# Kernel optimization log

Measured on AMD Instinct MI355X. Metric: run time of the kernel, lower is better.

The kernel has to match this reference:

```python
import jax, jax.numpy as jnp
import numpy as np

N_USERS = 100000
N_ITEMS = 50000
N_TOPICS = 1000
N_NODES = N_USERS + N_ITEMS + N_TOPICS
DIM = 64
LAYERS = 3
NNZ = 4000000
BATCH = 16384


def setup_inputs() -> dict:
    key = jax.random.key(0)
    ks = jax.random.split(key, 8)
    user_w = jax.random.normal(ks[0], (N_USERS, DIM), dtype=jnp.float32) * 0.1
    item_w = jax.random.normal(ks[1], (N_ITEMS, DIM), dtype=jnp.float32) * 0.1
    topic_w = jax.random.normal(ks[2], (N_TOPICS, DIM), dtype=jnp.float32) * 0.1
    vals = jax.random.uniform(ks[3], (NNZ,), dtype=jnp.float32)
    row = jax.random.randint(ks[4], (NNZ,), 0, N_NODES, dtype=jnp.int32)
    col = jax.random.randint(ks[5], (NNZ,), 0, N_NODES, dtype=jnp.int32)
    users = jax.random.randint(ks[6], (BATCH,), 0, N_USERS, dtype=jnp.int32)
    items = jax.random.randint(ks[7], (BATCH,), 0, N_ITEMS, dtype=jnp.int32)
    return {"user_w": user_w, "item_w": item_w, "topic_w": topic_w,
            "vals": vals, "row": row, "col": col,
            "users": users, "items": items}


def _spmm(vals, row, col, x):
    # y[r] = sum over edges e with row[e]==r of vals[e] * x[col[e]]
    msgs = vals[:, None] * x[col]  # [NNZ, DIM]
    return jax.ops.segment_sum(msgs, row, num_segments=N_NODES)


def reference(user_w, item_w, topic_w, vals, row, col, users, items):
    all_emb = jnp.concatenate([user_w, item_w, topic_w], axis=0)  # [N, D]
    acc = all_emb
    emb = all_emb
    for _ in range(LAYERS):
        emb = _spmm(vals, row, col, emb)
        acc = acc + emb
    out = acc / jnp.asarray(LAYERS + 1, dtype=acc.dtype)  # mean over stacked layers
    u = out[users]                       # [B, D] user rows
    i = out[N_USERS + items]             # [B, D] item rows (offset into node table)
    return jnp.sum(u * i, axis=1)        # [B]
```

## Files before the change

### kernel.cpp

```cpp
#include <hip/hip_runtime.h>
#include <hip/hip_fp16.h>

#define N_USERS 100000
#define N_ITEMS 50000
#define N_TOPICS 1000
#define N_NODES (N_USERS + N_ITEMS + N_TOPICS)
#define DIM 64
#define NNZ 4000000
#define BATCH 16384

#define BROWS 128
#define NB ((N_NODES + BROWS - 1) / BROWS)
#define NPART 256
#define CHUNK ((NNZ + NPART - 1) / NPART)
#define SEGCAP 4608

#define QSCALE 16384.0f
#define QINV   6.103515625e-05f

#define CONCAT_TOTAL (N_NODES * (DIM / 4))
#define CONCAT_BLOCKS ((CONCAT_TOTAL + 1023) / 1024)
#define BINIT_TOTAL (2 * BATCH * (DIM / 4))
#define BINIT_BLOCKS ((BINIT_TOTAL + 1023) / 1024)

__global__ void __launch_bounds__(1024)
phase0(const float4* __restrict__ uw,
       const float4* __restrict__ iw,
       const float4* __restrict__ tw,
       const int* __restrict__ row,
       const int* __restrict__ users,
       const int* __restrict__ items,
       __half2* __restrict__ x0,
       float4* __restrict__ accb,
       int* __restrict__ hcnt,
       int* __restrict__ sync) {
    __shared__ int h[NB];
    const int blk = blockIdx.x;
    const int t = threadIdx.x;
    if (blk < NPART) {
        if (blk == 0 && t == 0) *sync = 0;
        for (int i = t; i < NB; i += 1024) h[i] = 0;
        __syncthreads();
        int e0 = blk * CHUNK;
        int e1 = e0 + CHUNK; if (e1 > NNZ) e1 = NNZ;
        for (int e = e0 + t; e < e1; e += 1024) {
            int r = __builtin_nontemporal_load(&row[e]);
            atomicAdd(&h[r >> 7], 1);
        }
        __syncthreads();
        int* dst = hcnt + (size_t)blk * NB;
        for (int i = t; i < NB; i += 1024) dst[i] = h[i];
    } else if (blk < NPART + CONCAT_BLOCKS) {
        int tid = (blk - NPART) * 1024 + t;
        if (tid >= CONCAT_TOTAL) return;
        int node = tid >> 4;
        int q = tid & 15;
        float4 v;
        if (node < N_USERS)                v = uw[node * 16 + q];
        else if (node < N_USERS + N_ITEMS) v = iw[(node - N_USERS) * 16 + q];
        else                               v = tw[(node - N_USERS - N_ITEMS) * 16 + q];
        x0[tid * 2]     = __floats2half2_rn(v.x, v.y);
        x0[tid * 2 + 1] = __floats2half2_rn(v.z, v.w);
    } else {
        int tid = (blk - NPART - CONCAT_BLOCKS) * 1024 + t;
        if (tid >= BINIT_TOTAL) return;
        int r = tid >> 4;
        int q = tid & 15;
        float4 v;
        if (r < BATCH) v = uw[(size_t)users[r] * 16 + q];
        else           v = iw[(size_t)items[r - BATCH] * 16 + q];
        accb[tid] = v;
    }
}

__global__ void __launch_bounds__(256)
part_scanAB(int* __restrict__ hcnt,
            int* __restrict__ bcnt,
            int* __restrict__ bptr,
            int* __restrict__ rowptr,
            int* __restrict__ sync) {
    const int t = threadIdx.x;
    const int lane = t & 63;
    const int wid = t >> 6;
    int b = blockIdx.x * 4 + wid;
    int carry = 0;
    for (int base = 0; base < NPART; base += 64) {
        int g = base + lane;
        int v = hcnt[(size_t)g * NB + b];
        int x = v;
        #pragma unroll
        for (int off = 1; off < 64; off <<= 1) {
            int y = __shfl_up(x, off, 64);
            if (lane >= off) x += y;
        }
        int tot = __shfl(x, 63, 64);
        hcnt[(size_t)g * NB + b] = carry + x - v;
        carry += tot;
    }
    if (lane == 0) bcnt[b] = carry;
    __syncthreads();
    __threadfence();
    __shared__ int lastFlag;
    if (t == 0) lastFlag = (atomicAdd(sync, 1) == (int)gridDim.x - 1);
    __syncthreads();
    if (!lastFlag) return;

    __shared__ int wsum[4];
    __shared__ int carry_s;
    if (t == 0) carry_s = 0;
    __syncthreads();
    for (int base = 0; base < NB; base += 256) {
        int i = base + t;
        int v = (i < NB) ? bcnt[i] : 0;
        int x = v;
        #pragma unroll
        for (int off = 1; off < 64; off <<= 1) {
            int y = __shfl_up(x, off, 64);
            if (lane >= off) x += y;
        }
        if (lane == 63) wsum[wid] = x;
        __syncthreads();
        int wbase = 0;
        for (int w = 0; w < wid; ++w) wbase += wsum[w];
        int excl = carry_s + wbase + (x - v);
        if (i < NB) bptr[i] = excl;
        __syncthreads();
        if (t == 255) carry_s = excl + v;
        __syncthreads();
    }
    if (t == 0) { bptr[NB] = NNZ; rowptr[N_NODES] = NNZ; }
}

__global__ void __launch_bounds__(1024)
part_scatter(const int* __restrict__ row,
             const int* __restrict__ col,
             const float* __restrict__ vals,
             const int* __restrict__ hcnt,
             const int* __restrict__ bptr,
             int2* __restrict__ cvtmp) {
    __shared__ int cur[NB];
    const int g = blockIdx.x;
    const int t = threadIdx.x;
    const int* hoff = hcnt + (size_t)g * NB;
    for (int i = t; i < NB; i += 1024) cur[i] = bptr[i] + hoff[i];
    __syncthreads();
    int e0 = g * CHUNK;
    int e1 = e0 + CHUNK; if (e1 > NNZ) e1 = NNZ;
    for (int e = e0 + t; e < e1; e += 1024) {
        int r = __builtin_nontemporal_load(&row[e]);
        int c = __builtin_nontemporal_load(&col[e]);
        float v = __builtin_nontemporal_load(&vals[e]);
        int p = atomicAdd(&cur[r >> 7], 1);
        cvtmp[p] = make_int2(((r & (BROWS - 1)) << 18) | c, __float_as_int(v));
    }
}

__global__ void __launch_bounds__(256)
bucket_sort(const int* __restrict__ bptr,
            const long long* __restrict__ cvtmp,
            unsigned int* __restrict__ cv,
            int* __restrict__ rowptr) {
    __shared__ int2 seg[SEGCAP];
    __shared__ int cnt[BROWS];
    __shared__ int cur[BROWS];
    const int t = threadIdx.x;
    const int b = blockIdx.x;
    const int beg = bptr[b];
    const int end = bptr[b + 1];
    const int n = end - beg;

    for (int i = t; i < BROWS; i += 256) cnt[i] = 0;
    const bool lds_path = (n <= SEGCAP);

    if (lds_path) {
        for (int j = t; j < n; j += 256) {
            long long e = __builtin_nontemporal_load(&cvtmp[beg + j]);
            seg[j] = make_int2((int)e, (int)(e >> 32));
        }
    }
    __syncthreads();

    if (lds_path) {
        for (int j = t; j < n; j += 256)
            atomicAdd(&cnt[(seg[j].x >> 18) & (BROWS - 1)], 1);
    } else {
        for (int j = beg + t; j < end; j += 256) {
            long long e = cvtmp[j];
            atomicAdd(&cnt[((int)e >> 18) & (BROWS - 1)], 1);
        }
    }
    __syncthreads();

    if (t < 64) {
        int lane = t;
        int v0 = cnt[lane];
        int v1 = cnt[64 + lane];
        int x0 = v0;
        #pragma unroll
        for (int off = 1; off < 64; off <<= 1) {
            int y = __shfl_up(x0, off, 64);
            if (lane >= off) x0 += y;
        }
        int tot0 = __shfl(x0, 63, 64);
        int x1 = v1;
        #pragma unroll
        for (int off = 1; off < 64; off <<= 1) {
            int y = __shfl_up(x1, off, 64);
            if (lane >= off) x1 += y;
        }
        x1 += tot0;
        int e0 = x0 - v0;
        int e1 = x1 - v1;
        cur[lane] = e0;
        cur[64 + lane] = e1;
        int rowbase = b * BROWS;
        if (rowbase + lane < N_NODES)      rowptr[rowbase + lane] = beg + e0;
        if (rowbase + 64 + lane < N_NODES) rowptr[rowbase + 64 + lane] = beg + e1;
    }
    __syncthreads();

    if (lds_path) {
        for (int j = t; j < n; j += 256) {
            int2 e = seg[j];
            int p = atomicAdd(&cur[(e.x >> 18) & (BROWS - 1)], 1);
            float v = __int_as_float(e.y);
            unsigned int qv = (unsigned int)(v * QSCALE + 0.5f);
            if (qv > 16383u) qv = 16383u;
            cv[beg + p] = (qv << 18) | (unsigned int)(e.x & 0x3FFFF);
        }
    } else {
        for (int j = beg + t; j < end; j += 256) {
            long long e = cvtmp[j];
            int lo = (int)e;
            float v = __int_as_float((int)(e >> 32));
            int p = atomicAdd(&cur[(lo >> 18) & (BROWS - 1)], 1);
            unsigned int qv = (unsigned int)(v * QSCALE + 0.5f);
            if (qv > 16383u) qv = 16383u;
            cv[beg + p] = (qv << 18) | (unsigned int)(lo & 0x3FFFF);
        }
    }
}

__global__ void spmm_csr(const int* __restrict__ rowptr,
                         const unsigned int* __restrict__ cv,
                         const __half2* __restrict__ x2,
                         __half2* __restrict__ y2) {
    int bucket = blockIdx.x >> 4;
    int sub = blockIdx.x & 15;
    int lane = threadIdx.x & 63;
    int half = lane >> 5;
    int r = bucket * BROWS + sub * 8 + (threadIdx.x >> 6) * 2 + half;
    if (r >= N_NODES) return;
    int d = lane & 31;
    int beg = rowptr[r];
    int end = rowptr[r + 1];
    float ax = 0.0f, ay = 0.0f;
    int j = beg;
    for (; j + 15 < end; j += 16) {
        unsigned int u[16];
        __half2 h[16];
        #pragma unroll
        for (int k = 0; k < 16; ++k) u[k] = cv[j + k];
        #pragma unroll
        for (int k = 0; k < 16; ++k) h[k] = x2[(size_t)(u[k] & 0x3FFFF) * 32 + d];
        #pragma unroll
        for (int k = 0; k < 16; ++k) {
            float2 f = __half22float2(h[k]);
            float v = (float)(u[k] >> 18) * QINV;
            ax = fmaf(v, f.x, ax); ay = fmaf(v, f.y, ay);
        }
    }
    for (; j + 7 < end; j += 8) {
        unsigned int u[8];
        __half2 h[8];
        #pragma unroll
        for (int k = 0; k < 8; ++k) u[k] = cv[j + k];
        #pragma unroll
        for (int k = 0; k < 8; ++k) h[k] = x2[(size_t)(u[k] & 0x3FFFF) * 32 + d];
        #pragma unroll
        for (int k = 0; k < 8; ++k) {
            float2 f = __half22float2(h[k]);
            float v = (float)(u[k] >> 18) * QINV;
            ax = fmaf(v, f.x, ax); ay = fmaf(v, f.y, ay);
        }
    }
    for (; j + 3 < end; j += 4) {
        unsigned int u[4];
        __half2 h[4];
        #pragma unroll
        for (int k = 0; k < 4; ++k) u[k] = cv[j + k];
        #pragma unroll
        for (int k = 0; k < 4; ++k) h[k] = x2[(size_t)(u[k] & 0x3FFFF) * 32 + d];
        #pragma unroll
        for (int k = 0; k < 4; ++k) {
            float2 f = __half22float2(h[k]);
            float v = (float)(u[k] >> 18) * QINV;
            ax = fmaf(v, f.x, ax); ay = fmaf(v, f.y, ay);
        }
    }
    for (; j < end; ++j) {
        unsigned int u = cv[j];
        float2 f = __half22float2(x2[(size_t)(u & 0x3FFFF) * 32 + d]);
        float v = (float)(u >> 18) * QINV;
        ax = fmaf(v, f.x, ax); ay = fmaf(v, f.y, ay);
    }
    __half2 o = __floats2half2_rn(ax, ay);
    unsigned int ob;
    __builtin_memcpy(&ob, &o, 4);
    __builtin_nontemporal_store(ob, (unsigned int*)&y2[(size_t)r * 32 + d]);
}

__global__ void spmm_batch(const int* __restrict__ rowptr,
                           const unsigned int* __restrict__ cv,
                           const __half2* __restrict__ x2,
                           const int* __restrict__ users,
                           const int* __restrict__ items,
                           float* __restrict__ accb) {
    int lane = threadIdx.x & 63;
    int half = lane >> 5;
    int b = blockIdx.x * 8 + (threadIdx.x >> 6) * 2 + half;
    if (b >= 2 * BATCH) return;
    int d = lane & 31;
    int r = (b < BATCH) ? users[b] : (N_USERS + items[b - BATCH]);
    int beg = rowptr[r];
    int end = rowptr[r + 1];
    float ax = 0.0f, ay = 0.0f;
    int j = beg;
    for (; j + 15 < end; j += 16) {
        unsigned int u[16];
        __half2 h[16];
        #pragma unroll
        for (int k = 0; k < 16; ++k) u[k] = cv[j + k];
        #pragma unroll
        for (int k = 0; k < 16; ++k) h[k] = x2[(size_t)(u[k] & 0x3FFFF) * 32 + d];
        #pragma unroll
        for (int k = 0; k < 16; ++k) {
            float2 f = __half22float2(h[k]);
            float v = (float)(u[k] >> 18) * QINV;
            ax = fmaf(v, f.x, ax); ay = fmaf(v, f.y, ay);
        }
    }
    for (; j + 7 < end; j += 8) {
        unsigned int u[8];
        __half2 h[8];
        #pragma unroll
        for (int k = 0; k < 8; ++k) u[k] = cv[j + k];
        #pragma unroll
        for (int k = 0; k < 8; ++k) h[k] = x2[(size_t)(u[k] & 0x3FFFF) * 32 + d];
        #pragma unroll
        for (int k = 0; k < 8; ++k) {
            float2 f = __half22float2(h[k]);
            float v = (float)(u[k] >> 18) * QINV;
            ax = fmaf(v, f.x, ax); ay = fmaf(v, f.y, ay);
        }
    }
    for (; j + 3 < end; j += 4) {
        unsigned int u[4];
        __half2 h[4];
        #pragma unroll
        for (int k = 0; k < 4; ++k) u[k] = cv[j + k];
        #pragma unroll
        for (int k = 0; k < 4; ++k) h[k] = x2[(size_t)(u[k] & 0x3FFFF) * 32 + d];
        #pragma unroll
        for (int k = 0; k < 4; ++k) {
            float2 f = __half22float2(h[k]);
            float v = (float)(u[k] >> 18) * QINV;
            ax = fmaf(v, f.x, ax); ay = fmaf(v, f.y, ay);
        }
    }
    for (; j < end; ++j) {
        unsigned int u = cv[j];
        float2 f = __half22float2(x2[(size_t)(u & 0x3FFFF) * 32 + d]);
        float v = (float)(u >> 18) * QINV;
        ax = fmaf(v, f.x, ax); ay = fmaf(v, f.y, ay);
    }
    float2* a2 = (float2*)(accb + (size_t)b * 64 + 2 * d);
    float2 o = *a2;
    o.x += ax; o.y += ay;
    *a2 = o;
}

__global__ void batch_add(const __half* __restrict__ emb,
                          const int* __restrict__ users,
                          const int* __restrict__ items,
                          float4* __restrict__ accb) {
    int tid = blockIdx.x * blockDim.x + threadIdx.x;
    const int total = 2 * BATCH * (DIM / 4);
    if (tid >= total) return;
    int r = tid >> 4;
    int q = tid & 15;
    int node = (r < BATCH) ? users[r] : (N_USERS + items[r - BATCH]);
    const __half2* e2 = (const __half2*)(emb + (size_t)node * 64 + q * 4);
    float2 lo = __half22float2(e2[0]);
    float2 hi = __half22float2(e2[1]);
    float4 a = accb[tid];
    a.x += lo.x; a.y += lo.y; a.z += hi.x; a.w += hi.y;
    accb[tid] = a;
}

__global__ void final_dot(const float* __restrict__ accb,
                          float* __restrict__ out) {
    int b = blockIdx.x * 4 + (threadIdx.x >> 6);
    int lane = threadIdx.x & 63;
    if (b >= BATCH) return;
    float pu = accb[(size_t)b * 64 + lane];
    float pi = accb[(size_t)(BATCH + b) * 64 + lane];
    float p = pu * pi;
    #pragma unroll
    for (int off = 32; off > 0; off >>= 1)
        p += __shfl_down(p, off, 64);
    if (lane == 0) out[b] = p * (1.0f / 16.0f);
}

extern "C" void kernel_launch(void* const* d_in, const int* in_sizes, int n_in,
                              void* d_out, int out_size, void* d_ws, size_t ws_size,
                              hipStream_t stream) {
    const float* uw   = (const float*)d_in[0];
    const float* iw   = (const float*)d_in[1];
    const float* tw   = (const float*)d_in[2];
    const float* vals = (const float*)d_in[3];
    const int*   row  = (const int*)d_in[4];
    const int*   col  = (const int*)d_in[5];
    const int*   users= (const int*)d_in[6];
    const int*   items= (const int*)d_in[7];
    float* out = (float*)d_out;

    char* ws = (char*)d_ws;
    const size_t NODE_F = (size_t)N_NODES * DIM;
    __half* A     = (__half*)ws; ws += NODE_F * 2;
    __half* B     = (__half*)ws; ws += NODE_F * 2;
    float* ACCB   = (float*)ws;  ws += (size_t)2 * BATCH * DIM * 4;
    int*   bcnt   = (int*)ws;    ws += (size_t)NB * 4;
    int*   bptr   = (int*)ws;    ws += (size_t)(NB + 1) * 4;
    int*   rowptr = (int*)ws;    ws += (size_t)(N_NODES + 1) * 4;
    int*   hcnt   = (int*)ws;    ws += (size_t)NPART * NB * 4;
    int*   sync   = (int*)ws;    ws += 64;
    unsigned int* cv = (unsigned int*)ws; ws += (size_t)NNZ * 4;
    int2*  cvtmp  = (int2*)ws;   ws += (size_t)NNZ * 8;

    const int batch_v4 = 2 * BATCH * (DIM / 4);

    phase0<<<NPART + CONCAT_BLOCKS + BINIT_BLOCKS, 1024, 0, stream>>>(
        (const float4*)uw, (const float4*)iw, (const float4*)tw, row,
        users, items, (__half2*)A, (float4*)ACCB, hcnt, sync);

    part_scanAB<<<NB / 4, 256, 0, stream>>>(hcnt, bcnt, bptr, rowptr, sync);
    part_scatter<<<NPART, 1024, 0, stream>>>(row, col, vals, hcnt, bptr, cvtmp);
    bucket_sort<<<NB, 256, 0, stream>>>(bptr, (const long long*)cvtmp, cv, rowptr);

    const int spmm_blocks = NB * 16;
    spmm_csr<<<spmm_blocks, 256, 0, stream>>>(rowptr, cv, (const __half2*)A,
                                              (__half2*)B);
    batch_add<<<(batch_v4 + 255) / 256, 256, 0, stream>>>(
        B, users, items, (float4*)ACCB);
    spmm_csr<<<spmm_blocks, 256, 0, stream>>>(rowptr, cv, (const __half2*)B,
                                              (__half2*)A);
    batch_add<<<(batch_v4 + 255) / 256, 256, 0, stream>>>(
        A, users, items, (float4*)ACCB);
    spmm_batch<<<(2 * BATCH + 7) / 8, 256, 0, stream>>>(
        rowptr, cv, (const __half2*)A, users, items, ACCB);

    final_dot<<<(BATCH + 3) / 4, 256, 0, stream>>>(ACCB, out);
}
```

Before: 446.3 us.

## Locally bucket-sort edge sub-chunks in LDS before scattering to global

part_scatter now handles each partition in sub-chunks. Each sub-chunk is counted per bucket, prefix-scanned and scattered into an LDS buffer, then copied to cvtmp so that entries of the same bucket are written contiguously. The goal is to turn random 8-byte global writes into short runs that coalesce better. In exchange the row array is read twice, each element does a binary search, and there are extra block-wide scans and barriers. NPART is halved to 128, which gives fewer, longer-running blocks on the many-CU device and reduces parallelism.

```diff
diff --git a/kernel.cpp b/kernel.cpp
--- a/kernel.cpp
+++ b/kernel.cpp
@@ -11,8 +11,9 @@
 
 #define BROWS 128
 #define NB ((N_NODES + BROWS - 1) / BROWS)
-#define NPART 256
+#define NPART 128
 #define CHUNK ((NNZ + NPART - 1) / NPART)
+#define SUB 7813
 #define SEGCAP 4608
 
 #define QSCALE 16384.0f
@@ -138,20 +139,70 @@
              const int* __restrict__ hcnt,
              const int* __restrict__ bptr,
              int2* __restrict__ cvtmp) {
-    __shared__ int cur[NB];
+    __shared__ int2 sorted[SUB];
+    __shared__ int cnt_s[NB];
+    __shared__ int cur_s[NB];
+    __shared__ int gcur[NB];
+    __shared__ int wsum[16];
+    __shared__ int carry_s;
     const int g = blockIdx.x;
     const int t = threadIdx.x;
+    const int lane = t & 63;
+    const int wid = t >> 6;
     const int* hoff = hcnt + (size_t)g * NB;
-    for (int i = t; i < NB; i += 1024) cur[i] = bptr[i] + hoff[i];
-    __syncthreads();
+    for (int i = t; i < NB; i += 1024) gcur[i] = bptr[i] + hoff[i];
     int e0 = g * CHUNK;
     int e1 = e0 + CHUNK; if (e1 > NNZ) e1 = NNZ;
-    for (int e = e0 + t; e < e1; e += 1024) {
-        int r = __builtin_nontemporal_load(&row[e]);
-        int c = __builtin_nontemporal_load(&col[e]);
-        float v = __builtin_nontemporal_load(&vals[e]);
-        int p = atomicAdd(&cur[r >> 7], 1);
-        cvtmp[p] = make_int2(((r & (BROWS - 1)) << 18) | c, __float_as_int(v));
+
+    for (int s0 = e0; s0 < e1; s0 += SUB) {
+        int n = e1 - s0; if (n > SUB) n = SUB;
+        for (int i = t; i < NB; i += 1024) cnt_s[i] = 0;
+        if (t == 0) carry_s = 0;
+        __syncthreads();
+        for (int j = t; j < n; j += 1024) {
+            int r = __builtin_nontemporal_load(&row[s0 + j]);
+            atomicAdd(&cnt_s[r >> 7], 1);
+        }
+        __syncthreads();
+        for (int base = 0; base < NB; base += 1024) {
+            int i = base + t;
+            int v = (i < NB) ? cnt_s[i] : 0;
+            int x = v;
+            #pragma unroll
+            for (int off = 1; off < 64; off <<= 1) {
+                int y = __shfl_up(x, off, 64);
+                if (lane >= off) x += y;
+            }
+            if (lane == 63) wsum[wid] = x;
+            __syncthreads();
+            int wbase = 0;
+            for (int w = 0; w < wid; ++w) wbase += wsum[w];
+            int excl = carry_s + wbase + (x - v);
+            if (i < NB) cur_s[i] = excl;
+            __syncthreads();
+            if (t == 1023) carry_s = excl + v;
+            __syncthreads();
+        }
+        for (int j = t; j < n; j += 1024) {
+            int r = __builtin_nontemporal_load(&row[s0 + j]);
+            int c = __builtin_nontemporal_load(&col[s0 + j]);
+            float v = __builtin_nontemporal_load(&vals[s0 + j]);
+            int p = atomicAdd(&cur_s[r >> 7], 1);
+            sorted[p] = make_int2(((r & (BROWS - 1)) << 18) | c, __float_as_int(v));
+        }
+        __syncthreads();
+        for (int j = t; j < n; j += 1024) {
+            int lo = 0, hi = NB - 1;
+            while (lo < hi) {
+                int mid = (lo + hi) >> 1;
+                if (cur_s[mid] > j) hi = mid; else lo = mid + 1;
+            }
+            int lb = lo ? cur_s[lo - 1] : 0;
+            cvtmp[gcur[lo] + (j - lb)] = sorted[j];
+        }
+        __syncthreads();
+        for (int i = t; i < NB; i += 1024) gcur[i] += cnt_s[i];
+        __syncthreads();
     }
 }
 
```

Result: no change. 439.7 us (-1.5%).
